# Optimization experiments

Hardware: AMD Instinct MI355X
Metric: run time of the kernel (lower is better)

The kernel has to match this reference:

```python
import jax, jax.numpy as jnp
import numpy as np

NUM_HEADS = 32
NUM_KV_HEADS = 8
HEAD_DIM = 128  # hidden_size 4096 / 32 heads
ROPE_BASE = 10000.0


def setup_inputs() -> dict:
    key = jax.random.key(0)
    ks = jax.random.split(key, 5)
    H = NUM_HEADS * HEAD_DIM
    KV = NUM_KV_HEADS * HEAD_DIM
    B, S = 1, 2048
    s = 0.02
    return {
        "hidden_states": jax.random.normal(ks[0], (B, S, H), dtype=jnp.float32),
        "Wq": jax.random.normal(ks[1], (H, H), dtype=jnp.float32) * s,
        "Wk": jax.random.normal(ks[2], (H, KV), dtype=jnp.float32) * s,
        "Wv": jax.random.normal(ks[3], (H, KV), dtype=jnp.float32) * s,
        "Wo": jax.random.normal(ks[4], (H, H), dtype=jnp.float32) * s,
    }


def _rope_tables(seq_len, head_dim, dtype):
    inv_freq = 1.0 / (ROPE_BASE ** (jnp.arange(0, head_dim, 2, dtype=jnp.float32) / head_dim))
    freqs = jnp.arange(seq_len, dtype=jnp.float32)[:, None] * inv_freq[None, :]  # [S, hd/2]
    emb = jnp.concatenate([freqs, freqs], axis=-1)  # [S, hd]
    return emb.astype(dtype)  # angles; cos/sin taken by caller


def _rotate_half(x):
    x1, x2 = jnp.split(x, 2, axis=-1)
    return jnp.concatenate([-x2, x1], axis=-1)


def reference(hidden_states, Wq, Wk, Wv, Wo):
    B, S, H = hidden_states.shape
    hd = HEAD_DIM
    scale = hd ** -0.5

    q = (hidden_states @ Wq).reshape(B, S, NUM_HEADS, hd).transpose(0, 2, 1, 3)      # [B,nh,S,hd]
    k = (hidden_states @ Wk).reshape(B, S, NUM_KV_HEADS, hd).transpose(0, 2, 1, 3)   # [B,nkv,S,hd]
    v = (hidden_states @ Wv).reshape(B, S, NUM_KV_HEADS, hd).transpose(0, 2, 1, 3)

    ang = _rope_tables(S, hd, hidden_states.dtype)          # [S, hd]
    cos = jnp.cos(ang)[None, None]                          # [1,1,S,hd]
    sin = jnp.sin(ang)[None, None]
    q = q * cos + _rotate_half(q) * sin
    k = k * cos + _rotate_half(k) * sin

    rep = NUM_HEADS // NUM_KV_HEADS
    if rep > 1:
        k = jnp.repeat(k, rep, axis=1)  # matches torch repeat_interleave on head dim
        v = jnp.repeat(v, rep, axis=1)

    scores = jnp.einsum("bhqd,bhkd->bhqk", q, k) * scale    # [B,nh,S,S]
    causal = jnp.triu(jnp.ones((S, S), dtype=bool), k=1)
    scores = jnp.where(causal[None, None], jnp.float32(-jnp.inf).astype(scores.dtype), scores)
    weights = jax.nn.softmax(scores, axis=-1)
    attn = jnp.einsum("bhqk,bhkd->bhqd", weights, v)        # [B,nh,S,hd]
    out = attn.transpose(0, 2, 1, 3).reshape(B, S, H) @ Wo  # [B,S,H]
    return (out, k, v)
```

## Files before the change

### kernel.cpp

```cpp
#include <hip/hip_runtime.h>
#include <hip/hip_bf16.h>
#include <math.h>

typedef __bf16 bf16_t;
typedef bf16_t bf16x8 __attribute__((ext_vector_type(8)));
typedef bf16_t bf16x4 __attribute__((ext_vector_type(4)));
typedef float  f32x4  __attribute__((ext_vector_type(4)));

#define AS1(p) ((__attribute__((address_space(1))) void*)(p))
#define AS3(p) ((__attribute__((address_space(3))) void*)(p))

__global__ void convert_f32_bf16(const float* __restrict__ in, bf16_t* __restrict__ out)
{
    int i = blockIdx.x * 256 + threadIdx.x;
    float4 v = ((const float4*)in)[i];
    bf16x4 o;
    o[0] = (bf16_t)v.x; o[1] = (bf16_t)v.y; o[2] = (bf16_t)v.z; o[3] = (bf16_t)v.w;
    ((bf16x4*)out)[i] = o;
}

__global__ void transpose_convert(const float* __restrict__ W, bf16_t* __restrict__ Wt,
                                  int K, int N)
{
    __shared__ float tile[32][33];
    const int n0 = blockIdx.x * 32;
    const int k0 = blockIdx.y * 32;
    const int r = threadIdx.x >> 5;
    const int c = threadIdx.x & 31;
    #pragma unroll
    for (int i = 0; i < 32; i += 8)
        tile[r + i][c] = W[(size_t)(k0 + r + i) * N + n0 + c];
    __syncthreads();
    #pragma unroll
    for (int i = 0; i < 32; i += 8)
        Wt[(size_t)(n0 + r + i) * K + k0 + c] = (bf16_t)tile[c][r + i];
}

template <typename OutT>
__global__ __launch_bounds__(256)
void gemm_bt_128(const bf16_t* __restrict__ A, const bf16_t* __restrict__ Bt,
                 OutT* __restrict__ C, int M, int N, int K)
{
    __shared__ bf16_t As[128 * 32];
    __shared__ bf16_t Bs[128 * 32];
    const int t    = threadIdx.x;
    const int lane = t & 63;
    const int wave = t >> 6;
    const int m0 = blockIdx.x * 128;
    const int n0 = blockIdx.y * 128;
    const int wm = (wave & 1) * 64;
    const int wn = (wave >> 1) * 64;
    const int lm = lane & 15;
    const int lq = lane >> 4;

    f32x4 acc[4][4] = {};

    const int chunk0 = wave * 64 + lane;
    const int r0 = chunk0 >> 2, c0 = (chunk0 & 3) * 8;
    const int chunk1 = 256 + chunk0;
    const int r1 = chunk1 >> 2, c1 = (chunk1 & 3) * 8;

    const bf16_t* Ag0 = A  + (size_t)(m0 + r0) * K + c0;
    const bf16_t* Ag1 = A  + (size_t)(m0 + r1) * K + c1;
    const bf16_t* Bg0 = Bt + (size_t)(n0 + r0) * K + c0;
    const bf16_t* Bg1 = Bt + (size_t)(n0 + r1) * K + c1;
    bf16_t* As0 = As + (wave * 64) * 8;
    bf16_t* As1 = As + (256 + wave * 64) * 8;
    bf16_t* Bs0 = Bs + (wave * 64) * 8;
    bf16_t* Bs1 = Bs + (256 + wave * 64) * 8;

    for (int k0 = 0; k0 < K; k0 += 32) {
        __syncthreads();
        __builtin_amdgcn_global_load_lds(AS1(Ag0 + k0), AS3(As0), 16, 0, 0);
        __builtin_amdgcn_global_load_lds(AS1(Ag1 + k0), AS3(As1), 16, 0, 0);
        __builtin_amdgcn_global_load_lds(AS1(Bg0 + k0), AS3(Bs0), 16, 0, 0);
        __builtin_amdgcn_global_load_lds(AS1(Bg1 + k0), AS3(Bs1), 16, 0, 0);
        __syncthreads();

        bf16x8 af[4], bb[4];
        #pragma unroll
        for (int mt = 0; mt < 4; ++mt)
            af[mt] = *(const bf16x8*)(As + (wm + mt * 16 + lm) * 32 + lq * 8);
        #pragma unroll
        for (int nt = 0; nt < 4; ++nt)
            bb[nt] = *(const bf16x8*)(Bs + (wn + nt * 16 + lm) * 32 + lq * 8);
        #pragma unroll
        for (int mt = 0; mt < 4; ++mt)
            #pragma unroll
            for (int nt = 0; nt < 4; ++nt)
                acc[mt][nt] = __builtin_amdgcn_mfma_f32_16x16x32_bf16(
                    af[mt], bb[nt], acc[mt][nt], 0, 0, 0);
    }

    #pragma unroll
    for (int mt = 0; mt < 4; ++mt) {
        #pragma unroll
        for (int nt = 0; nt < 4; ++nt) {
            const int row = m0 + wm + mt * 16 + lq * 4;
            const int col = n0 + wn + nt * 16 + lm;
            #pragma unroll
            for (int r = 0; r < 4; ++r) {
                float v = acc[mt][nt][r];
                if constexpr (sizeof(OutT) == 2)
                    C[(size_t)(row + r) * N + col] = (OutT)(bf16_t)v;
                else
                    C[(size_t)(row + r) * N + col] = v;
            }
        }
    }
}

__global__ void rope_qk(bf16_t* __restrict__ QKV, float* __restrict__ k_out, int S)
{
    int idx  = blockIdx.x * 256 + threadIdx.x;
    int d    = idx & 63;
    int s    = idx >> 6;
    int head = blockIdx.y;
    float ang = (float)s * exp2f((float)d * -0.20762050593f);
    float sn, cs;
    sincosf(ang, &sn, &cs);
    int col = head < 32 ? head * 128 : 4096 + (head - 32) * 128;
    bf16_t* p = QKV + (size_t)s * 6144 + col;
    float x1 = (float)p[d], x2 = (float)p[d + 64];
    float y1 = x1 * cs - x2 * sn;
    float y2 = x2 * cs + x1 * sn;
    p[d]      = (bf16_t)y1;
    p[d + 64] = (bf16_t)y2;
    if (head >= 32) {
        int g = head - 32;
        #pragma unroll
        for (int j = 0; j < 4; ++j) {
            float* kb = k_out + ((size_t)(g * 4 + j) * S + s) * 128;
            kb[d]      = y1;
            kb[d + 64] = y2;
        }
    }
}

__global__ void v_finish(const bf16_t* __restrict__ QKV, float* __restrict__ v_out,
                         bf16_t* __restrict__ Vt, int S)
{
    __shared__ bf16_t tl[32][33];
    const int s0  = blockIdx.x * 32;
    const int gd0 = blockIdx.y * 32;
    const int r = threadIdx.x >> 5;
    const int c = threadIdx.x & 31;
    #pragma unroll
    for (int i = 0; i < 32; i += 8) {
        int s = s0 + r + i;
        bf16_t v = QKV[(size_t)s * 6144 + 5120 + gd0 + c];
        tl[r + i][c] = v;
        int gd = gd0 + c;
        int g = gd >> 7, d = gd & 127;
        float vf = (float)v;
        #pragma unroll
        for (int j = 0; j < 4; ++j)
            v_out[((size_t)(g * 4 + j) * S + s) * 128 + d] = vf;
    }
    __syncthreads();
    #pragma unroll
    for (int i = 0; i < 32; i += 8)
        Vt[(size_t)(gd0 + r + i) * S + s0 + c] = tl[c][r + i];
}

__global__ void pack_frags(const bf16_t* __restrict__ QKV, const bf16_t* __restrict__ Vt,
                           bf16_t* __restrict__ Kfrag, bf16_t* __restrict__ Vfrag, int S)
{
    const int b  = blockIdx.x;
    const int g  = b >> 5, kt = b & 31;
    const int t  = threadIdx.x;
    bf16x8* Kf = (bf16x8*)Kfrag + (size_t)b * 1024;
    bf16x8* Vf = (bf16x8*)Vfrag + (size_t)b * 1024;
    #pragma unroll
    for (int i = 0; i < 4; ++i) {
        int slot = i * 256 + t;
        int f = slot >> 6, l = slot & 63;
        int kk = f >> 2, nt = f & 3, lm = l & 15, lq = l >> 4;
        Kf[slot] = *(const bf16x8*)(QKV + (size_t)(kt * 64 + nt * 16 + lm) * 6144
                                    + 4096 + g * 128 + kk * 32 + lq * 8);
    }
    #pragma unroll
    for (int i = 0; i < 4; ++i) {
        int slot = i * 256 + t;
        int f = slot >> 6, l = slot & 63;
        int kk = f >> 3, nt = f & 7, lm = l & 15, lq = l >> 4;
        Vf[slot] = *(const bf16x8*)(Vt + (size_t)(g * 128 + nt * 16 + lm) * S
                                    + kt * 64 + kk * 32 + lq * 8);
    }
}

__global__ __launch_bounds__(64, 2)
void attn_fwd(const bf16_t* __restrict__ QKV,
              const bf16_t* __restrict__ Kfrag, const bf16_t* __restrict__ Vfrag,
              bf16_t* __restrict__ O, int S)
{
    const int task = blockIdx.x;
    const int h    = task & 31;
    const int c    = 63 - (task >> 5);
    const int g    = h >> 2;
    const int lane = threadIdx.x;
    const int lm   = lane & 15;
    const int lq   = lane >> 4;
    const int q0   = c * 32;

    __shared__ bf16_t P[32 * 72];

    bf16x8 aq[2][4];
    #pragma unroll
    for (int mi = 0; mi < 2; ++mi) {
        const bf16_t* qrow = QKV + (size_t)(q0 + mi * 16 + lm) * 6144 + h * 128;
        #pragma unroll
        for (int kk = 0; kk < 4; ++kk)
            aq[mi][kk] = *(const bf16x8*)(qrow + kk * 32 + lq * 8);
    }

    f32x4 acc[2][8] = {};
    float mrow[2][4], lrow[2][4];
    #pragma unroll
    for (int mi = 0; mi < 2; ++mi)
        #pragma unroll
        for (int r = 0; r < 4; ++r) { mrow[mi][r] = -3.0e38f; lrow[mi][r] = 0.f; }
    const float scale = 0.08838834764831845f;

    const int nkt = (q0 >> 6) + 1;

    for (int kt = 0; kt < nkt; ++kt) {
        const int k0 = kt * 64;
        const bf16x8* Kf = (const bf16x8*)Kfrag + ((size_t)(g * 32 + kt) << 10);
        const bf16x8* Vf = (const bf16x8*)Vfrag + ((size_t)(g * 32 + kt) << 10);

        bf16x8 bk[4][4];
        #pragma unroll
        for (int kk = 0; kk < 4; ++kk)
            #pragma unroll
            for (int nt = 0; nt < 4; ++nt)
                bk[kk][nt] = Kf[(kk * 4 + nt) * 64 + lane];

        f32x4 sc[2][4] = {};
        #pragma unroll
        for (int kk = 0; kk < 4; ++kk)
            #pragma unroll
            for (int nt = 0; nt < 4; ++nt)
                #pragma unroll
                for (int mi = 0; mi < 2; ++mi)
                    sc[mi][nt] = __builtin_amdgcn_mfma_f32_16x16x32_bf16(
                        aq[mi][kk], bk[kk][nt], sc[mi][nt], 0, 0, 0);

        bf16x8 bv[2][8];
        #pragma unroll
        for (int kk = 0; kk < 2; ++kk)
            #pragma unroll
            for (int nt = 0; nt < 8; ++nt)
                bv[kk][nt] = Vf[(kk * 8 + nt) * 64 + lane];

        #pragma unroll
        for (int mi = 0; mi < 2; ++mi)
            #pragma unroll
            for (int nt = 0; nt < 4; ++nt)
                #pragma unroll
                for (int r = 0; r < 4; ++r)
                    sc[mi][nt][r] *= scale;

        if (kt == nkt - 1) {
            #pragma unroll
            for (int mi = 0; mi < 2; ++mi)
                #pragma unroll
                for (int nt = 0; nt < 4; ++nt) {
                    int col = k0 + nt * 16 + lm;
                    #pragma unroll
                    for (int r = 0; r < 4; ++r) {
                        int row = q0 + mi * 16 + lq * 4 + r;
                        if (col > row) sc[mi][nt][r] = -3.0e38f;
                    }
                }
        }

        #pragma unroll
        for (int mi = 0; mi < 2; ++mi) {
            float tmax[4];
            #pragma unroll
            for (int r = 0; r < 4; ++r)
                tmax[r] = fmaxf(fmaxf(sc[mi][0][r], sc[mi][1][r]),
                                fmaxf(sc[mi][2][r], sc[mi][3][r]));
            #pragma unroll
            for (int off = 1; off < 16; off <<= 1)
                #pragma unroll
                for (int r = 0; r < 4; ++r)
                    tmax[r] = fmaxf(tmax[r], __shfl_xor(tmax[r], off));

            float alpha[4];
            #pragma unroll
            for (int r = 0; r < 4; ++r) {
                float mn = fmaxf(mrow[mi][r], tmax[r]);
                alpha[r] = __expf(mrow[mi][r] - mn);
                mrow[mi][r] = mn;
            }
            float rsum[4] = {0.f, 0.f, 0.f, 0.f};
            #pragma unroll
            for (int nt = 0; nt < 4; ++nt)
                #pragma unroll
                for (int r = 0; r < 4; ++r) {
                    float p = __expf(sc[mi][nt][r] - mrow[mi][r]);
                    sc[mi][nt][r] = p;
                    rsum[r] += p;
                }
            #pragma unroll
            for (int off = 1; off < 16; off <<= 1)
                #pragma unroll
                for (int r = 0; r < 4; ++r)
                    rsum[r] += __shfl_xor(rsum[r], off);
            #pragma unroll
            for (int r = 0; r < 4; ++r)
                lrow[mi][r] = lrow[mi][r] * alpha[r] + rsum[r];
            #pragma unroll
            for (int nt = 0; nt < 8; ++nt)
                #pragma unroll
                for (int r = 0; r < 4; ++r)
                    acc[mi][nt][r] *= alpha[r];

            #pragma unroll
            for (int nt = 0; nt < 4; ++nt)
                #pragma unroll
                for (int r = 0; r < 4; ++r)
                    P[(mi * 16 + lq * 4 + r) * 72 + nt * 16 + lm] = (bf16_t)sc[mi][nt][r];
        }

        bf16x8 ap[2][2];
        #pragma unroll
        for (int mi = 0; mi < 2; ++mi)
            #pragma unroll
            for (int kk = 0; kk < 2; ++kk)
                ap[mi][kk] = *(const bf16x8*)(P + (mi * 16 + lm) * 72 + kk * 32 + lq * 8);

        #pragma unroll
        for (int kk = 0; kk < 2; ++kk)
            #pragma unroll
            for (int nt = 0; nt < 8; ++nt)
                #pragma unroll
                for (int mi = 0; mi < 2; ++mi)
                    acc[mi][nt] = __builtin_amdgcn_mfma_f32_16x16x32_bf16(
                        ap[mi][kk], bv[kk][nt], acc[mi][nt], 0, 0, 0);
    }

    #pragma unroll
    for (int mi = 0; mi < 2; ++mi) {
        float inv[4];
        #pragma unroll
        for (int r = 0; r < 4; ++r) inv[r] = 1.0f / lrow[mi][r];
        #pragma unroll
        for (int nt = 0; nt < 8; ++nt)
            #pragma unroll
            for (int r = 0; r < 4; ++r) {
                int row = q0 + mi * 16 + lq * 4 + r;
                O[(size_t)row * 4096 + h * 128 + nt * 16 + lm] =
                    (bf16_t)(acc[mi][nt][r] * inv[r]);
            }
    }
}

extern "C" void kernel_launch(void* const* d_in, const int* in_sizes, int n_in,
                              void* d_out, int out_size, void* d_ws, size_t ws_size,
                              hipStream_t stream)
{
    const float* hidden = (const float*)d_in[0];
    const float* Wq = (const float*)d_in[1];
    const float* Wk = (const float*)d_in[2];
    const float* Wv = (const float*)d_in[3];
    const float* Wo = (const float*)d_in[4];

    const int S = 2048, H = 4096, KV = 1024, NQKV = 6144;

    char* ws = (char*)d_ws;
    bf16_t* hid_b  = (bf16_t*)(ws);
    bf16_t* Wqkv_t = (bf16_t*)(ws + (size_t)(16u  << 20));
    bf16_t* Wo_t   = (bf16_t*)(ws + (size_t)(64u  << 20));
    bf16_t* QKV    = (bf16_t*)(ws + (size_t)(96u  << 20));
    bf16_t* Vt     = (bf16_t*)(ws + (size_t)(120u << 20));
    bf16_t* attn   = (bf16_t*)(ws + (size_t)(124u << 20));
    bf16_t* Kfrag  = (bf16_t*)(ws);
    bf16_t* Vfrag  = (bf16_t*)(ws + (size_t)(4u << 20));

    float* out_o = (float*)d_out;
    float* out_k = out_o + (size_t)S * H;
    float* out_v = out_k + (size_t)32 * S * 128;

    convert_f32_bf16<<<S * H / 4 / 256, 256, 0, stream>>>(hidden, hid_b);
    transpose_convert<<<dim3(H / 32, H / 32), 256, 0, stream>>>(Wq, Wqkv_t, H, H);
    transpose_convert<<<dim3(KV / 32, H / 32), 256, 0, stream>>>(Wk, Wqkv_t + (size_t)4096 * H, H, KV);
    transpose_convert<<<dim3(KV / 32, H / 32), 256, 0, stream>>>(Wv, Wqkv_t + (size_t)5120 * H, H, KV);
    transpose_convert<<<dim3(H / 32, H / 32), 256, 0, stream>>>(Wo, Wo_t, H, H);

    gemm_bt_128<bf16_t><<<dim3(S / 128, NQKV / 128), 256, 0, stream>>>(hid_b, Wqkv_t, QKV, S, NQKV, H);

    rope_qk<<<dim3(S * 64 / 256, 40), 256, 0, stream>>>(QKV, out_k, S);
    v_finish<<<dim3(S / 32, KV / 32), 256, 0, stream>>>(QKV, out_v, Vt, S);
    pack_frags<<<256, 256, 0, stream>>>(QKV, Vt, Kfrag, Vfrag, S);

    attn_fwd<<<2048, 64, 0, stream>>>(QKV, Kfrag, Vfrag, attn, S);

    gemm_bt_128<float><<<dim3(S / 128, H / 128), 256, 0, stream>>>(attn, Wo_t, out_o, S, H, H);
}
```

Measured before the change: 630.0 us.

## Replace 128x128 GEMM with double-buffered 256x256 tile, swizzled LDS kernel

Replaces the single-buffered 128x128x32 GEMM with a 512-thread 256x256x64 tile kernel. It uses double-buffered LDS filled by direct global-to-LDS loads and an XOR swizzle to avoid bank conflicts. The loop is split into four MFMA quadrants with interleaved prefetch, barriers and setprio, aiming for more data reuse and for global loads to overlap compute. The larger tile yields fewer blocks: 8x24=192 for QKV and 8x16=128 for the output projection, so the output projection in particular may underfill the CUs.

After: 660.7 us. 1.05x slower.

```diff
diff --git a/kernel.cpp b/kernel.cpp
--- a/kernel.cpp
+++ b/kernel.cpp
@@ -37,70 +37,157 @@
 }
 
 template <typename OutT>
-__global__ __launch_bounds__(256)
-void gemm_bt_128(const bf16_t* __restrict__ A, const bf16_t* __restrict__ Bt,
+__global__ __launch_bounds__(512, 2)
+void gemm_bt_256(const bf16_t* __restrict__ A, const bf16_t* __restrict__ Bt,
                  OutT* __restrict__ C, int M, int N, int K)
 {
-    __shared__ bf16_t As[128 * 32];
-    __shared__ bf16_t Bs[128 * 32];
-    const int t    = threadIdx.x;
-    const int lane = t & 63;
-    const int wave = t >> 6;
-    const int m0 = blockIdx.x * 128;
-    const int n0 = blockIdx.y * 128;
-    const int wm = (wave & 1) * 64;
-    const int wn = (wave >> 1) * 64;
-    const int lm = lane & 15;
-    const int lq = lane >> 4;
-
-    f32x4 acc[4][4] = {};
-
-    const int chunk0 = wave * 64 + lane;
-    const int r0 = chunk0 >> 2, c0 = (chunk0 & 3) * 8;
-    const int chunk1 = 256 + chunk0;
-    const int r1 = chunk1 >> 2, c1 = (chunk1 & 3) * 8;
-
-    const bf16_t* Ag0 = A  + (size_t)(m0 + r0) * K + c0;
-    const bf16_t* Ag1 = A  + (size_t)(m0 + r1) * K + c1;
-    const bf16_t* Bg0 = Bt + (size_t)(n0 + r0) * K + c0;
-    const bf16_t* Bg1 = Bt + (size_t)(n0 + r1) * K + c1;
-    bf16_t* As0 = As + (wave * 64) * 8;
-    bf16_t* As1 = As + (256 + wave * 64) * 8;
-    bf16_t* Bs0 = Bs + (wave * 64) * 8;
-    bf16_t* Bs1 = Bs + (256 + wave * 64) * 8;
-
-    for (int k0 = 0; k0 < K; k0 += 32) {
-        __syncthreads();
-        __builtin_amdgcn_global_load_lds(AS1(Ag0 + k0), AS3(As0), 16, 0, 0);
-        __builtin_amdgcn_global_load_lds(AS1(Ag1 + k0), AS3(As1), 16, 0, 0);
-        __builtin_amdgcn_global_load_lds(AS1(Bg0 + k0), AS3(Bs0), 16, 0, 0);
-        __builtin_amdgcn_global_load_lds(AS1(Bg1 + k0), AS3(Bs1), 16, 0, 0);
-        __syncthreads();
-
-        bf16x8 af[4], bb[4];
-        #pragma unroll
-        for (int mt = 0; mt < 4; ++mt)
-            af[mt] = *(const bf16x8*)(As + (wm + mt * 16 + lm) * 32 + lq * 8);
-        #pragma unroll
-        for (int nt = 0; nt < 4; ++nt)
-            bb[nt] = *(const bf16x8*)(Bs + (wn + nt * 16 + lm) * 32 + lq * 8);
-        #pragma unroll
-        for (int mt = 0; mt < 4; ++mt)
-            #pragma unroll
-            for (int nt = 0; nt < 4; ++nt)
-                acc[mt][nt] = __builtin_amdgcn_mfma_f32_16x16x32_bf16(
-                    af[mt], bb[nt], acc[mt][nt], 0, 0, 0);
-    }
-
-    #pragma unroll
-    for (int mt = 0; mt < 4; ++mt) {
-        #pragma unroll
-        for (int nt = 0; nt < 4; ++nt) {
-            const int row = m0 + wm + mt * 16 + lq * 4;
-            const int col = n0 + wn + nt * 16 + lm;
+    __shared__ __align__(16) bf16_t As[2 * 256 * 64];
+    __shared__ __align__(16) bf16_t Bs[2 * 256 * 64];
+
+    const int tid  = threadIdx.x;
+    const int wave = tid >> 6;
+    const int lane = tid & 63;
+    const int lm = lane & 15, lq = lane >> 4;
+    const int wr = wave >> 2, wc = wave & 3;
+    const int m0 = blockIdx.x * 256;
+    const int n0 = blockIdx.y * 256;
+
+    const int sr = tid >> 3;
+    const int sg = ((tid & 7) ^ (sr & 7)) * 8;
+    char* Ab = (char*)As;
+    char* Bb = (char*)Bs;
+    const int fl = lm * 128 + ((lq ^ (lm & 7)) << 4);
+
+    const int NT = K >> 6;
+
+#define STAGE_A(buf, kt, h) do {                                                              \
+    const bf16_t* _g0 = A + (size_t)(m0 + (h) * 128 + sr) * K + (kt) * 64 + sg;               \
+    const bf16_t* _g1 = A + (size_t)(m0 + (h) * 128 + 64 + sr) * K + (kt) * 64 + sg;          \
+    __builtin_amdgcn_global_load_lds(AS1(_g0),                                                \
+        AS3(Ab + (buf) * 32768 + ((h) * 128 + wave * 8) * 128), 16, 0, 0);                    \
+    __builtin_amdgcn_global_load_lds(AS1(_g1),                                                \
+        AS3(Ab + (buf) * 32768 + ((h) * 128 + 64 + wave * 8) * 128), 16, 0, 0);               \
+} while (0)
+#define STAGE_B(buf, kt, h) do {                                                              \
+    const bf16_t* _g0 = Bt + (size_t)(n0 + (h) * 128 + sr) * K + (kt) * 64 + sg;              \
+    const bf16_t* _g1 = Bt + (size_t)(n0 + (h) * 128 + 64 + sr) * K + (kt) * 64 + sg;         \
+    __builtin_amdgcn_global_load_lds(AS1(_g0),                                                \
+        AS3(Bb + (buf) * 32768 + ((h) * 128 + wave * 8) * 128), 16, 0, 0);                    \
+    __builtin_amdgcn_global_load_lds(AS1(_g1),                                                \
+        AS3(Bb + (buf) * 32768 + ((h) * 128 + 64 + wave * 8) * 128), 16, 0, 0);               \
+} while (0)
+
+    f32x4 acc[8][4] = {};
+
+    STAGE_A(0, 0, 0); STAGE_A(0, 0, 1);
+    STAGE_B(0, 0, 0); STAGE_B(0, 0, 1);
+    if (NT > 1) STAGE_A(1, 1, 0);
+    asm volatile("s_waitcnt vmcnt(2)" ::: "memory");
+    __builtin_amdgcn_s_barrier();
+
+    int cur = 0;
+    for (int kt = 0; kt < NT; ++kt) {
+        const int nxt = cur ^ 1;
+        const char* Ac = Ab + cur * 32768;
+        const char* Bc = Bb + cur * 32768;
+        bf16x8 a0[4][2], a1[4][2], b0[2][2], b1[2][2];
+
+        #pragma unroll
+        for (int mf = 0; mf < 4; ++mf)
+            #pragma unroll
+            for (int kk = 0; kk < 2; ++kk)
+                a0[mf][kk] = *(const bf16x8*)(Ac + (wr * 128 + mf * 16) * 128 + (fl ^ (kk << 6)));
+        #pragma unroll
+        for (int nf = 0; nf < 2; ++nf)
+            #pragma unroll
+            for (int kk = 0; kk < 2; ++kk)
+                b0[nf][kk] = *(const bf16x8*)(Bc + (wc * 64 + nf * 16) * 128 + (fl ^ (kk << 6)));
+        if (kt + 1 < NT) { STAGE_A(nxt, kt + 1, 1); STAGE_B(nxt, kt + 1, 0); }
+        __builtin_amdgcn_s_barrier();
+        asm volatile("s_waitcnt lgkmcnt(0)" ::: "memory");
+        __builtin_amdgcn_s_setprio(1);
+        #pragma unroll
+        for (int mf = 0; mf < 4; ++mf)
+            #pragma unroll
+            for (int nf = 0; nf < 2; ++nf)
+                #pragma unroll
+                for (int kk = 0; kk < 2; ++kk)
+                    acc[mf][nf] = __builtin_amdgcn_mfma_f32_16x16x32_bf16(
+                        a0[mf][kk], b0[nf][kk], acc[mf][nf], 0, 0, 0);
+        __builtin_amdgcn_s_setprio(0);
+        __builtin_amdgcn_s_barrier();
+
+        #pragma unroll
+        for (int nf = 0; nf < 2; ++nf)
+            #pragma unroll
+            for (int kk = 0; kk < 2; ++kk)
+                b1[nf][kk] = *(const bf16x8*)(Bc + (wc * 64 + 32 + nf * 16) * 128 + (fl ^ (kk << 6)));
+        if (kt + 1 < NT) STAGE_B(nxt, kt + 1, 1);
+        __builtin_amdgcn_s_barrier();
+        asm volatile("s_waitcnt lgkmcnt(0)" ::: "memory");
+        __builtin_amdgcn_s_setprio(1);
+        #pragma unroll
+        for (int mf = 0; mf < 4; ++mf)
+            #pragma unroll
+            for (int nf = 0; nf < 2; ++nf)
+                #pragma unroll
+                for (int kk = 0; kk < 2; ++kk)
+                    acc[mf][2 + nf] = __builtin_amdgcn_mfma_f32_16x16x32_bf16(
+                        a0[mf][kk], b1[nf][kk], acc[mf][2 + nf], 0, 0, 0);
+        __builtin_amdgcn_s_setprio(0);
+        __builtin_amdgcn_s_barrier();
+
+        #pragma unroll
+        for (int mf = 0; mf < 4; ++mf)
+            #pragma unroll
+            for (int kk = 0; kk < 2; ++kk)
+                a1[mf][kk] = *(const bf16x8*)(Ac + (wr * 128 + 64 + mf * 16) * 128 + (fl ^ (kk << 6)));
+        __builtin_amdgcn_s_barrier();
+        asm volatile("s_waitcnt lgkmcnt(0)" ::: "memory");
+        __builtin_amdgcn_s_setprio(1);
+        #pragma unroll
+        for (int mf = 0; mf < 4; ++mf)
+            #pragma unroll
+            for (int nf = 0; nf < 2; ++nf)
+                #pragma unroll
+                for (int kk = 0; kk < 2; ++kk)
+                    acc[4 + mf][nf] = __builtin_amdgcn_mfma_f32_16x16x32_bf16(
+                        a1[mf][kk], b0[nf][kk], acc[4 + mf][nf], 0, 0, 0);
+        __builtin_amdgcn_s_setprio(0);
+        __builtin_amdgcn_s_barrier();
+
+        if (kt + 2 < NT) {
+            STAGE_A(cur, kt + 2, 0);
+            asm volatile("s_waitcnt vmcnt(2)" ::: "memory");
+        } else {
+            asm volatile("s_waitcnt vmcnt(0)" ::: "memory");
+        }
+        __builtin_amdgcn_s_barrier();
+        __builtin_amdgcn_s_setprio(1);
+        #pragma unroll
+        for (int mf = 0; mf < 4; ++mf)
+            #pragma unroll
+            for (int nf = 0; nf < 2; ++nf)
+                #pragma unroll
+                for (int kk = 0; kk < 2; ++kk)
+                    acc[4 + mf][2 + nf] = __builtin_amdgcn_mfma_f32_16x16x32_bf16(
+                        a1[mf][kk], b1[nf][kk], acc[4 + mf][2 + nf], 0, 0, 0);
+        __builtin_amdgcn_s_setprio(0);
+        __builtin_amdgcn_s_barrier();
+        cur = nxt;
+    }
+#undef STAGE_A
+#undef STAGE_B
+
+    #pragma unroll
+    for (int mi = 0; mi < 8; ++mi) {
+        #pragma unroll
+        for (int ni = 0; ni < 4; ++ni) {
+            const int row = m0 + wr * 128 + mi * 16 + lq * 4;
+            const int col = n0 + wc * 64 + ni * 16 + lm;
             #pragma unroll
             for (int r = 0; r < 4; ++r) {
-                float v = acc[mt][nt][r];
+                float v = acc[mi][ni][r];
                 if constexpr (sizeof(OutT) == 2)
                     C[(size_t)(row + r) * N + col] = (OutT)(bf16_t)v;
                 else
@@ -390,7 +477,7 @@
     transpose_convert<<<dim3(KV / 32, H / 32), 256, 0, stream>>>(Wv, Wqkv_t + (size_t)5120 * H, H, KV);
     transpose_convert<<<dim3(H / 32, H / 32), 256, 0, stream>>>(Wo, Wo_t, H, H);
 
-    gemm_bt_128<bf16_t><<<dim3(S / 128, NQKV / 128), 256, 0, stream>>>(hid_b, Wqkv_t, QKV, S, NQKV, H);
+    gemm_bt_256<bf16_t><<<dim3(S / 256, NQKV / 256), 512, 0, stream>>>(hid_b, Wqkv_t, QKV, S, NQKV, H);
 
     rope_qk<<<dim3(S * 64 / 256, 40), 256, 0, stream>>>(QKV, out_k, S);
     v_finish<<<dim3(S / 32, KV / 32), 256, 0, stream>>>(QKV, out_v, Vt, S);
@@ -398,5 +485,5 @@
 
     attn_fwd<<<2048, 64, 0, stream>>>(QKV, Kfrag, Vfrag, attn, S);
 
-    gemm_bt_128<float><<<dim3(S / 128, H / 128), 256, 0, stream>>>(attn, Wo_t, out_o, S, H, H);
-}
+    gemm_bt_256<float><<<dim3(S / 256, H / 256), 512, 0, stream>>>(attn, Wo_t, out_o, S, H, H);
+}
```

## Pre-pack GEMM A operands in MFMA fragment layout and load directly to registers

Applied to the files above, without the earlier changes.

The hidden-state conversion and the attention epilogue now write their outputs in a fragment-packed layout that matches the MFMA A-operand lane mapping. Both GEMMs read A fragments straight from global memory into registers instead of staging them through LDS. This halves LDS traffic and global-to-LDS loads per k-step. In exchange, A reuse across the two waves that share the same rows now comes from cache rather than shared memory, and the attention epilogue gains an LDS round-trip to produce the packed layout.

Result: slower. 698.7 us (+10.9%).

```diff
diff --git a/kernel.cpp b/kernel.cpp
--- a/kernel.cpp
+++ b/kernel.cpp
@@ -10,13 +10,20 @@
 #define AS1(p) ((__attribute__((address_space(1))) void*)(p))
 #define AS3(p) ((__attribute__((address_space(3))) void*)(p))
 
-__global__ void convert_f32_bf16(const float* __restrict__ in, bf16_t* __restrict__ out)
-{
-    int i = blockIdx.x * 256 + threadIdx.x;
-    float4 v = ((const float4*)in)[i];
-    bf16x4 o;
-    o[0] = (bf16_t)v.x; o[1] = (bf16_t)v.y; o[2] = (bf16_t)v.z; o[3] = (bf16_t)v.w;
-    ((bf16x4*)out)[i] = o;
+__global__ void convert_pack(const float* __restrict__ in, bf16_t* __restrict__ Af)
+{
+    int slot = blockIdx.x * 256 + threadIdx.x;
+    int l    = slot & 63;
+    int ks   = (slot >> 6) & 127;
+    int r16  = slot >> 13;
+    int row  = r16 * 16 + (l & 15);
+    int col  = ks * 32 + (l >> 4) * 8;
+    const float4* p = (const float4*)(in + (size_t)row * 4096 + col);
+    float4 v0 = p[0], v1 = p[1];
+    bf16x8 o;
+    o[0] = (bf16_t)v0.x; o[1] = (bf16_t)v0.y; o[2] = (bf16_t)v0.z; o[3] = (bf16_t)v0.w;
+    o[4] = (bf16_t)v1.x; o[5] = (bf16_t)v1.y; o[6] = (bf16_t)v1.z; o[7] = (bf16_t)v1.w;
+    ((bf16x8*)Af)[slot] = o;
 }
 
 __global__ void transpose_convert(const float* __restrict__ W, bf16_t* __restrict__ Wt,
@@ -38,10 +45,9 @@
 
 template <typename OutT>
 __global__ __launch_bounds__(256)
-void gemm_bt_128(const bf16_t* __restrict__ A, const bf16_t* __restrict__ Bt,
-                 OutT* __restrict__ C, int M, int N, int K)
-{
-    __shared__ bf16_t As[128 * 32];
+void gemm_af(const bf16_t* __restrict__ Af, const bf16_t* __restrict__ Bt,
+             OutT* __restrict__ C, int M, int N, int K)
+{
     __shared__ bf16_t Bs[128 * 32];
     const int t    = threadIdx.x;
     const int lane = t & 63;
@@ -52,6 +58,7 @@
     const int wn = (wave >> 1) * 64;
     const int lm = lane & 15;
     const int lq = lane >> 4;
+    const int K32 = K >> 5;
 
     f32x4 acc[4][4] = {};
 
@@ -60,27 +67,25 @@
     const int chunk1 = 256 + chunk0;
     const int r1 = chunk1 >> 2, c1 = (chunk1 & 3) * 8;
 
-    const bf16_t* Ag0 = A  + (size_t)(m0 + r0) * K + c0;
-    const bf16_t* Ag1 = A  + (size_t)(m0 + r1) * K + c1;
     const bf16_t* Bg0 = Bt + (size_t)(n0 + r0) * K + c0;
     const bf16_t* Bg1 = Bt + (size_t)(n0 + r1) * K + c1;
-    bf16_t* As0 = As + (wave * 64) * 8;
-    bf16_t* As1 = As + (256 + wave * 64) * 8;
     bf16_t* Bs0 = Bs + (wave * 64) * 8;
     bf16_t* Bs1 = Bs + (256 + wave * 64) * 8;
 
+    const bf16x8* Afr = (const bf16x8*)Af + ((size_t)((m0 + wm) >> 4) * K32) * 64 + lane;
+
     for (int k0 = 0; k0 < K; k0 += 32) {
         __syncthreads();
-        __builtin_amdgcn_global_load_lds(AS1(Ag0 + k0), AS3(As0), 16, 0, 0);
-        __builtin_amdgcn_global_load_lds(AS1(Ag1 + k0), AS3(As1), 16, 0, 0);
         __builtin_amdgcn_global_load_lds(AS1(Bg0 + k0), AS3(Bs0), 16, 0, 0);
         __builtin_amdgcn_global_load_lds(AS1(Bg1 + k0), AS3(Bs1), 16, 0, 0);
+        bf16x8 af[4];
+        const int ks = k0 >> 5;
+        #pragma unroll
+        for (int mt = 0; mt < 4; ++mt)
+            af[mt] = Afr[((size_t)mt * K32 + ks) * 64];
         __syncthreads();
 
-        bf16x8 af[4], bb[4];
-        #pragma unroll
-        for (int mt = 0; mt < 4; ++mt)
-            af[mt] = *(const bf16x8*)(As + (wm + mt * 16 + lm) * 32 + lq * 8);
+        bf16x8 bb[4];
         #pragma unroll
         for (int nt = 0; nt < 4; ++nt)
             bb[nt] = *(const bf16x8*)(Bs + (wn + nt * 16 + lm) * 32 + lq * 8);
@@ -192,7 +197,7 @@
 __global__ __launch_bounds__(64, 2)
 void attn_fwd(const bf16_t* __restrict__ QKV,
               const bf16_t* __restrict__ Kfrag, const bf16_t* __restrict__ Vfrag,
-              bf16_t* __restrict__ O, int S)
+              bf16_t* __restrict__ Of, int S)
 {
     const int task = blockIdx.x;
     const int h    = task & 31;
@@ -203,7 +208,8 @@
     const int lq   = lane >> 4;
     const int q0   = c * 32;
 
-    __shared__ bf16_t P[32 * 72];
+    __shared__ bf16_t smem[32 * 136];
+    bf16_t* P = smem;
 
     bf16x8 aq[2][4];
     #pragma unroll
@@ -342,6 +348,7 @@
                         ap[mi][kk], bv[kk][nt], acc[mi][nt], 0, 0, 0);
     }
 
+    bf16_t* EP = smem;
     #pragma unroll
     for (int mi = 0; mi < 2; ++mi) {
         float inv[4];
@@ -350,12 +357,18 @@
         #pragma unroll
         for (int nt = 0; nt < 8; ++nt)
             #pragma unroll
-            for (int r = 0; r < 4; ++r) {
-                int row = q0 + mi * 16 + lq * 4 + r;
-                O[(size_t)row * 4096 + h * 128 + nt * 16 + lm] =
+            for (int r = 0; r < 4; ++r)
+                EP[(mi * 16 + lq * 4 + r) * 136 + nt * 16 + lm] =
                     (bf16_t)(acc[mi][nt][r] * inv[r]);
-            }
-    }
+    }
+    bf16x8* O8 = (bf16x8*)Of;
+    #pragma unroll
+    for (int mi = 0; mi < 2; ++mi)
+        #pragma unroll
+        for (int j = 0; j < 4; ++j) {
+            bf16x8 gr = *(const bf16x8*)(EP + (mi * 16 + lm) * 136 + (j * 4 + lq) * 8);
+            O8[((size_t)((q0 >> 4) + mi) * 128 + h * 4 + j) * 64 + lane] = gr;
+        }
 }
 
 extern "C" void kernel_launch(void* const* d_in, const int* in_sizes, int n_in,
@@ -371,12 +384,12 @@
     const int S = 2048, H = 4096, KV = 1024, NQKV = 6144;
 
     char* ws = (char*)d_ws;
-    bf16_t* hid_b  = (bf16_t*)(ws);
+    bf16_t* APack  = (bf16_t*)(ws);
     bf16_t* Wqkv_t = (bf16_t*)(ws + (size_t)(16u  << 20));
     bf16_t* Wo_t   = (bf16_t*)(ws + (size_t)(64u  << 20));
     bf16_t* QKV    = (bf16_t*)(ws + (size_t)(96u  << 20));
     bf16_t* Vt     = (bf16_t*)(ws + (size_t)(120u << 20));
-    bf16_t* attn   = (bf16_t*)(ws + (size_t)(124u << 20));
+    bf16_t* OPack  = (bf16_t*)(ws + (size_t)(124u << 20));
     bf16_t* Kfrag  = (bf16_t*)(ws);
     bf16_t* Vfrag  = (bf16_t*)(ws + (size_t)(4u << 20));
 
@@ -384,19 +397,19 @@
     float* out_k = out_o + (size_t)S * H;
     float* out_v = out_k + (size_t)32 * S * 128;
 
-    convert_f32_bf16<<<S * H / 4 / 256, 256, 0, stream>>>(hidden, hid_b);
+    convert_pack<<<S * H / 8 / 256, 256, 0, stream>>>(hidden, APack);
     transpose_convert<<<dim3(H / 32, H / 32), 256, 0, stream>>>(Wq, Wqkv_t, H, H);
     transpose_convert<<<dim3(KV / 32, H / 32), 256, 0, stream>>>(Wk, Wqkv_t + (size_t)4096 * H, H, KV);
     transpose_convert<<<dim3(KV / 32, H / 32), 256, 0, stream>>>(Wv, Wqkv_t + (size_t)5120 * H, H, KV);
     transpose_convert<<<dim3(H / 32, H / 32), 256, 0, stream>>>(Wo, Wo_t, H, H);
 
-    gemm_bt_128<bf16_t><<<dim3(S / 128, NQKV / 128), 256, 0, stream>>>(hid_b, Wqkv_t, QKV, S, NQKV, H);
+    gemm_af<bf16_t><<<dim3(S / 128, NQKV / 128), 256, 0, stream>>>(APack, Wqkv_t, QKV, S, NQKV, H);
 
     rope_qk<<<dim3(S * 64 / 256, 40), 256, 0, stream>>>(QKV, out_k, S);
     v_finish<<<dim3(S / 32, KV / 32), 256, 0, stream>>>(QKV, out_v, Vt, S);
     pack_frags<<<256, 256, 0, stream>>>(QKV, Vt, Kfrag, Vfrag, S);
 
-    attn_fwd<<<2048, 64, 0, stream>>>(QKV, Kfrag, Vfrag, attn, S);
-
-    gemm_bt_128<float><<<dim3(S / 128, H / 128), 256, 0, stream>>>(attn, Wo_t, out_o, S, H, H);
-}
+    attn_fwd<<<2048, 64, 0, stream>>>(QKV, Kfrag, Vfrag, OPack, S);
+
+    gemm_af<float><<<dim3(S / 128, H / 128), 256, 0, stream>>>(OPack, Wo_t, out_o, S, H, H);
+}
```

## Split attention KV loop across four waves with LDS split-softmax merge

Applied to the files above, without the earlier changes.

Each attention block now runs four waves. The waves take interleaved KV tiles, each keeping its own online-softmax state, and the partial results are merged through shared memory: global max, rescaled sums, and serial accumulation of the output tiles. The goal is to shorten the long serial KV loop for late query chunks and raise parallelism per block. The cost is extra LDS traffic, several block-wide barriers in the epilogue, idle waves on early chunks that have fewer than four KV tiles, and higher register pressure under the new launch bounds.

Result: slower. 899.3 us (+42.7%).

```diff
diff --git a/kernel.cpp b/kernel.cpp
--- a/kernel.cpp
+++ b/kernel.cpp
@@ -189,7 +189,7 @@
     }
 }
 
-__global__ __launch_bounds__(64, 2)
+__global__ __launch_bounds__(256, 4)
 void attn_fwd(const bf16_t* __restrict__ QKV,
               const bf16_t* __restrict__ Kfrag, const bf16_t* __restrict__ Vfrag,
               bf16_t* __restrict__ O, int S)
@@ -198,12 +198,16 @@
     const int h    = task & 31;
     const int c    = 63 - (task >> 5);
     const int g    = h >> 2;
-    const int lane = threadIdx.x;
+    const int wave = threadIdx.x >> 6;
+    const int lane = threadIdx.x & 63;
     const int lm   = lane & 15;
     const int lq   = lane >> 4;
     const int q0   = c * 32;
 
-    __shared__ bf16_t P[32 * 72];
+    __shared__ __align__(16) char smem[18432];
+    bf16_t* P  = (bf16_t*)smem + wave * (32 * 72);
+    float*  Cb = (float*)smem;
+    float*  ml = (float*)(smem + 16896);
 
     bf16x8 aq[2][4];
     #pragma unroll
@@ -224,7 +228,7 @@
 
     const int nkt = (q0 >> 6) + 1;
 
-    for (int kt = 0; kt < nkt; ++kt) {
+    for (int kt = wave; kt < nkt; kt += 4) {
         const int k0 = kt * 64;
         const bf16x8* Kf = (const bf16x8*)Kfrag + ((size_t)(g * 32 + kt) << 10);
         const bf16x8* Vf = (const bf16x8*)Vfrag + ((size_t)(g * 32 + kt) << 10);
@@ -342,19 +346,65 @@
                         ap[mi][kk], bv[kk][nt], acc[mi][nt], 0, 0, 0);
     }
 
-    #pragma unroll
-    for (int mi = 0; mi < 2; ++mi) {
-        float inv[4];
-        #pragma unroll
-        for (int r = 0; r < 4; ++r) inv[r] = 1.0f / lrow[mi][r];
-        #pragma unroll
-        for (int nt = 0; nt < 8; ++nt)
+    if (lm == 0) {
+        #pragma unroll
+        for (int mi = 0; mi < 2; ++mi)
             #pragma unroll
             for (int r = 0; r < 4; ++r) {
-                int row = q0 + mi * 16 + lq * 4 + r;
-                O[(size_t)row * 4096 + h * 128 + nt * 16 + lm] =
-                    (bf16_t)(acc[mi][nt][r] * inv[r]);
+                int lr = mi * 16 + lq * 4 + r;
+                ml[(wave * 2 + 0) * 32 + lr] = mrow[mi][r];
+                ml[(wave * 2 + 1) * 32 + lr] = lrow[mi][r];
             }
+    }
+    __syncthreads();
+
+    float fac[2][4], linv[2][4];
+    #pragma unroll
+    for (int mi = 0; mi < 2; ++mi)
+        #pragma unroll
+        for (int r = 0; r < 4; ++r) {
+            int lr = mi * 16 + lq * 4 + r;
+            float m0 = ml[0 * 32 + lr], m1 = ml[2 * 32 + lr];
+            float m2 = ml[4 * 32 + lr], m3 = ml[6 * 32 + lr];
+            float mg = fmaxf(fmaxf(m0, m1), fmaxf(m2, m3));
+            float ls = ml[1 * 32 + lr] * __expf(m0 - mg)
+                     + ml[3 * 32 + lr] * __expf(m1 - mg)
+                     + ml[5 * 32 + lr] * __expf(m2 - mg)
+                     + ml[7 * 32 + lr] * __expf(m3 - mg);
+            fac[mi][r]  = __expf(mrow[mi][r] - mg);
+            linv[mi][r] = 1.0f / ls;
+        }
+
+    for (int w = 0; w < 3; ++w) {
+        if (wave == w) {
+            #pragma unroll
+            for (int mi = 0; mi < 2; ++mi)
+                #pragma unroll
+                for (int nt = 0; nt < 8; ++nt)
+                    #pragma unroll
+                    for (int r = 0; r < 4; ++r) {
+                        int lr = mi * 16 + lq * 4 + r;
+                        int col = nt * 16 + lm;
+                        float v = acc[mi][nt][r] * fac[mi][r];
+                        if (w == 0) Cb[lr * 132 + col] = v;
+                        else        Cb[lr * 132 + col] += v;
+                    }
+        }
+        __syncthreads();
+    }
+    if (wave == 3) {
+        #pragma unroll
+        for (int mi = 0; mi < 2; ++mi)
+            #pragma unroll
+            for (int nt = 0; nt < 8; ++nt)
+                #pragma unroll
+                for (int r = 0; r < 4; ++r) {
+                    int lr = mi * 16 + lq * 4 + r;
+                    int col = nt * 16 + lm;
+                    float v = Cb[lr * 132 + col] + acc[mi][nt][r] * fac[mi][r];
+                    O[(size_t)(q0 + lr) * 4096 + h * 128 + col] =
+                        (bf16_t)(v * linv[mi][r]);
+                }
     }
 }
 
@@ -396,7 +446,7 @@
     v_finish<<<dim3(S / 32, KV / 32), 256, 0, stream>>>(QKV, out_v, Vt, S);
     pack_frags<<<256, 256, 0, stream>>>(QKV, Vt, Kfrag, Vfrag, S);
 
-    attn_fwd<<<2048, 64, 0, stream>>>(QKV, Kfrag, Vfrag, attn, S);
+    attn_fwd<<<2048, 256, 0, stream>>>(QKV, Kfrag, Vfrag, attn, S);
 
     gemm_bt_128<float><<<dim3(S / 128, H / 128), 256, 0, stream>>>(attn, Wo_t, out_o, S, H, H);
 }
```
